# Performance work log

Hardware: AMD Instinct MI355X
Metric: run time of the kernel (lower is better)

Reference implementation:

```python
import jax, jax.numpy as jnp
import numpy as np
from jax import lax

LOG2PI = float(np.log(2.0 * np.pi))
N_K, N_T, N_C, N_D, N_SPK = 256, 128, 32, 10, 1000000

def _std_normal_logpdf(x):
    return -0.5 * (x * x + LOG2PI)

def _normal_logpdf(x, mu, log_sig):
    z = (x - mu) * jnp.exp(-log_sig)
    return -0.5 * (z * z + LOG2PI) - log_sig

def safe_log(x, minval=1e-10):
    return jnp.log(x + minval)

def setup_inputs() -> dict:
    key = jax.random.key(0)
    ks_ = jax.random.split(key, 8)
    s = jax.random.normal(ks_[0], (N_SPK, N_D), dtype=jnp.float32)
    y = jax.random.normal(ks_[1], (N_K, N_T), dtype=jnp.float32)
    ks = jax.random.randint(ks_[2], (N_SPK,), 0, N_K, dtype=jnp.int32)
    ts = jax.random.randint(ks_[3], (N_SPK,), 0, N_T, dtype=jnp.int32)
    means = jax.random.normal(ks_[4], (N_C, N_D), dtype=jnp.float32)
    A = jax.random.normal(ks_[5], (N_C, N_D, N_D), dtype=jnp.float32)
    covs = jnp.einsum('cij,ckj->cik', A, A) / N_D + jnp.eye(N_D, dtype=jnp.float32)
    b_mu = jax.random.normal(ks_[6], (N_C,), dtype=jnp.float32)
    b_log_sig = jax.random.normal(ks_[7], (N_C,), dtype=jnp.float32)
    beta_mu = jax.random.normal(jax.random.fold_in(key, 10), (N_C, N_T), dtype=jnp.float32)
    beta_log_sig = jax.random.normal(jax.random.fold_in(key, 11), (N_C, N_T), dtype=jnp.float32)
    return {"s": s, "y": y, "ks": ks, "ts": ts, "means": means, "covs": covs,
            "b_mu": b_mu, "b_log_sig": b_log_sig, "beta_mu": beta_mu, "beta_log_sig": beta_log_sig}

def _mvn_ll(s, means, covs):
    # ll[n, c] = MVN(means[c], covs[c]).log_prob(s[n]); loop over small n_c via lax.map
    L = jnp.linalg.cholesky(covs)                       # (c, d, d)
    logdet = 2.0 * jnp.sum(jnp.log(jnp.diagonal(L, axis1=1, axis2=2)), axis=1)  # (c,)
    d = s.shape[1]
    def comp(args):
        mu, Lc, ld = args
        diff = s - mu                                   # (n, d)
        z = jax.scipy.linalg.solve_triangular(Lc, diff.T, lower=True)  # (d, n)
        return -0.5 * (d * LOG2PI + ld + jnp.sum(z * z, axis=0))       # (n,)
    return lax.map(comp, (means, L, logdet)).T          # (n, c)

def reference(s, y, ks, ts, means, covs, b_mu, b_log_sig, beta_mu, beta_log_sig):
    # sampling=False path: use variational means
    b_sample, beta_sample = b_mu, beta_mu               # (c,), (c, t)
    # log_lambdas[k, c, t] = b[c] + beta[c, t] * y[k, t]
    log_lambdas = b_sample[None, :, None] + beta_sample[None, :, :] * y[:, None, :]
    log_pis = jax.nn.log_softmax(log_lambdas, axis=1)   # (k, c, t)
    ll = _mvn_ll(s, means, covs)                        # (n, c)
    logits = ll + log_pis[ks, :, ts]                    # per-spike gather -> (n, c)
    r = jax.nn.softmax(logits, axis=1)                  # responsibilities (n, c)
    log_prior = jnp.sum(_std_normal_logpdf(b_sample)) + jnp.sum(_std_normal_logpdf(beta_sample))
    log_q = jnp.sum(_normal_logpdf(b_sample, b_mu, b_log_sig)) + \
            jnp.sum(_normal_logpdf(beta_sample, beta_mu, beta_log_sig))
    elbo = log_prior - log_q
    elbo += jnp.sum(r * logits)
    elbo -= jnp.sum(r * safe_log(r))
    return elbo
```

## Files before the change

### kernel.cpp

```cpp
#include <hip/hip_runtime.h>
#include <hip/hip_bf16.h>
#include <math.h>

#define NK 256
#define NT 128
#define NC 32
#define ND 10
#define NSPK 1000000
#define LOG2PI 1.8378770664093453f
#define NCHUNK ((NSPK + 255) / 256)
#define GRID 1024

#define FSTR 36
#define LDS_DW (256 * FSTR)

typedef __attribute__((ext_vector_type(8))) short short8;
typedef __attribute__((ext_vector_type(4))) float floatx4;
typedef __attribute__((ext_vector_type(4))) int intx4;

union FragCvt { intx4 i; short8 s; };


__device__ inline unsigned pack_bf16(float a, float b) {
  __hip_bfloat16 ha = __float2bfloat16(a), hb = __float2bfloat16(b);
  unsigned short ua, ub;
  __builtin_memcpy(&ua, &ha, 2);
  __builtin_memcpy(&ub, &hb, 2);
  return (unsigned)ua | ((unsigned)ub << 16);
}

__global__ void prep_kernel(const float* __restrict__ y,
                            const float* __restrict__ means,
                            const float* __restrict__ covs,
                            const float* __restrict__ b_mu,
                            const float* __restrict__ b_ls,
                            const float* __restrict__ beta_mu,
                            const float* __restrict__ beta_ls,
                            int* __restrict__ wt,
                            float* __restrict__ cpack,
                            float* __restrict__ pisT,
                            double* __restrict__ acc,
                            unsigned int* __restrict__ counter) {
  int blk = blockIdx.x;
  int tid = threadIdx.x;

  if (blk == 0) {
    int c = tid;
    if (c >= NC) return;

    float M[ND][ND];
    #pragma unroll
    for (int i = 0; i < ND; ++i)
      #pragma unroll
      for (int j = 0; j < ND; ++j)
        M[i][j] = covs[c * ND * ND + i * ND + j];

    float logdet = 0.f;
    #pragma unroll
    for (int j = 0; j < ND; ++j) {
      float d = M[j][j];
      #pragma unroll
      for (int k = 0; k < ND; ++k) if (k < j) d -= M[j][k] * M[j][k];
      float sq = sqrtf(d);
      M[j][j] = sq;
      logdet += 2.f * __logf(sq);
      float inv = 1.f / sq;
      #pragma unroll
      for (int i = 0; i < ND; ++i) {
        if (i > j) {
          float s2 = M[i][j];
          #pragma unroll
          for (int k = 0; k < ND; ++k) if (k < j) s2 -= M[i][k] * M[j][k];
          M[i][j] = s2 * inv;
        }
      }
    }

    #pragma unroll
    for (int j = 0; j < ND; ++j) {
      M[j][j] = 1.f / M[j][j];
      #pragma unroll
      for (int i = 0; i < ND; ++i) {
        if (i > j) {
          float s2 = 0.f;
          #pragma unroll
          for (int k = 0; k < ND; ++k) if (k >= j && k < i) s2 += M[i][k] * M[k][j];
          M[i][j] = -s2 / M[i][i];
        }
      }
    }

    float pd[ND];
    #pragma unroll
    for (int i = 0; i < ND; ++i) {
      #pragma unroll
      for (int jj = 0; jj < ND; ++jj) {
        if (jj >= i) {
          float s2 = 0.f;
          #pragma unroll
          for (int k = 0; k < ND; ++k) if (k >= jj) s2 += M[k][i] * M[k][jj];
          if (jj > i) M[i][jj] = s2;
          else pd[i] = s2;
        }
      }
    }

    float mu[ND], q[ND];
    #pragma unroll
    for (int i = 0; i < ND; ++i) mu[i] = means[c * ND + i];
    float muPmu = 0.f;
    #pragma unroll
    for (int i = 0; i < ND; ++i) {
      float a2 = pd[i] * mu[i];
      #pragma unroll
      for (int j = 0; j < ND; ++j) {
        if (j < i) a2 += M[j][i] * mu[j];
        if (j > i) a2 += M[i][j] * mu[j];
      }
      q[i] = a2;
      muPmu += mu[i] * a2;
    }
    float cst = -0.5f * ((float)ND * LOG2PI + logdet + muPmu);

    float wv[64];
    int p = 0;
    #pragma unroll
    for (int i = 0; i < ND; ++i)
      #pragma unroll
      for (int j = 0; j < ND; ++j)
        if (j >= i && !(i == 9 && j == 9))
          wv[p++] = (i == j) ? -0.5f * pd[i] : -M[i][j];
    #pragma unroll
    for (int i = 0; i < ND; ++i) wv[54 + i] = q[i];

    #pragma unroll
    for (int j = 0; j < 32; ++j) {
      float a = wv[2 * j], b = wv[2 * j + 1];
      float ah = __bfloat162float(__float2bfloat16(a));
      float bh = __bfloat162float(__float2bfloat16(b));
      wt[c * 32 + j] = (int)pack_bf16(ah, bh);
      wt[(32 + c) * 32 + j] = (int)pack_bf16(a - ah, b - bh);
    }
    cpack[c] = cst;
    cpack[32 + c] = -0.5f * pd[9];

  } else if (blk == 1) {
    float local = 0.f;
    for (int i = tid; i < NC; i += 256)
      local += fmaf(-0.5f * b_mu[i], b_mu[i], b_ls[i]);
    for (int i = tid; i < NC * NT; i += 256)
      local += fmaf(-0.5f * beta_mu[i], beta_mu[i], beta_ls[i]);
    #pragma unroll
    for (int off = 32; off > 0; off >>= 1) local += __shfl_down(local, off);
    __shared__ float red[4];
    if ((tid & 63) == 0) red[tid >> 6] = local;
    __syncthreads();
    if (tid == 0) {
      acc[0] = (double)(red[0] + red[1] + red[2] + red[3]);
      counter[0] = 0u;
    }

  } else {
    int id = (blk - 2) * 256 + tid;
    int t = id & (NT - 1);
    float yv = y[id];
    float v[NC];
    float m = -1e30f;
    #pragma unroll
    for (int c = 0; c < NC; ++c) {
      v[c] = fmaf(beta_mu[c * NT + t], yv, b_mu[c]);
      m = fmaxf(m, v[c]);
    }
    float ssum = 0.f;
    #pragma unroll
    for (int c = 0; c < NC; ++c) ssum += __expf(v[c] - m);
    float lz = m + __logf(ssum);
    float* outp = pisT + (size_t)id * NC;
    #pragma unroll
    for (int c = 0; c < NC; ++c) outp[c] = v[c] - lz;
  }
}

__global__ __launch_bounds__(256, 4)
void spike_kernel(const float* __restrict__ s,
                  const int* __restrict__ ks,
                  const int* __restrict__ ts,
                  const int* __restrict__ wt,
                  const float* __restrict__ cpack,
                  const float* __restrict__ pisT,
                  double* __restrict__ acc,
                  unsigned int* __restrict__ counter,
                  float* __restrict__ out) {
  __shared__ int lds[LDS_DW];
  __shared__ float red[4];

  int tid = threadIdx.x;
  int wv_ = tid >> 6, L = tid & 63;
  int r = L & 15, q = L >> 4;

  FragCvt bf[2][2][2];
  #pragma unroll
  for (int h = 0; h < 2; ++h)
    #pragma unroll
    for (int nt = 0; nt < 2; ++nt)
      #pragma unroll
      for (int ks2 = 0; ks2 < 2; ++ks2)
        bf[h][nt][ks2].i =
            *(const intx4*)&wt[(h * 32 + nt * 16 + r) * 32 + ks2 * 16 + q * 4];

  float lse_sum = 0.f;

  for (int ci = blockIdx.x; ci < NCHUNK; ci += GRID) {
    int n = ci * 256 + tid;
    int nc = n < NSPK ? n : (NSPK - 1);

    const float2* srow = (const float2*)(s + (size_t)nc * ND);
    float sv[ND];
    #pragma unroll
    for (int i = 0; i < 5; ++i) {
      float2 v2 = srow[i];
      sv[2 * i] = v2.x;
      sv[2 * i + 1] = v2.y;
    }
    int kk_ = ks[nc], tt_ = ts[nc];

    float fv[64];
    {
      int p = 0;
      #pragma unroll
      for (int i = 0; i < ND; ++i)
        #pragma unroll
        for (int j = 0; j < ND; ++j)
          if (j >= i && !(i == 9 && j == 9)) fv[p++] = sv[i] * sv[j];
      #pragma unroll
      for (int i = 0; i < ND; ++i) fv[54 + i] = sv[i];
    }

    __syncthreads();
    {
      int rb = tid * FSTR;
      #pragma unroll
      for (int ch = 0; ch < 8; ++ch) {
        intx4 v;
        v.x = (int)pack_bf16(fv[8 * ch + 0], fv[8 * ch + 1]);
        v.y = (int)pack_bf16(fv[8 * ch + 2], fv[8 * ch + 3]);
        v.z = (int)pack_bf16(fv[8 * ch + 4], fv[8 * ch + 5]);
        v.w = (int)pack_bf16(fv[8 * ch + 6], fv[8 * ch + 7]);
        *(intx4*)&lds[rb + ch * 4] = v;
      }
    }
    __syncthreads();

    floatx4 accf[4][2];
    #pragma unroll
    for (int mt = 0; mt < 4; ++mt)
      #pragma unroll
      for (int nt = 0; nt < 2; ++nt)
        accf[mt][nt] = (floatx4){0.f, 0.f, 0.f, 0.f};

    #pragma unroll
    for (int mt = 0; mt < 4; ++mt) {
      #pragma unroll
      for (int ks2 = 0; ks2 < 2; ++ks2) {
        FragCvt a;
        a.i = *(const intx4*)&lds[(wv_ * 64 + mt * 16 + r) * FSTR + ks2 * 16 + q * 4];
        #pragma unroll
        for (int nt = 0; nt < 2; ++nt) {
          accf[mt][nt] = __builtin_amdgcn_mfma_f32_16x16x32_bf16(
              a.s, bf[0][nt][ks2].s, accf[mt][nt], 0, 0, 0);
          accf[mt][nt] = __builtin_amdgcn_mfma_f32_16x16x32_bf16(
              a.s, bf[1][nt][ks2].s, accf[mt][nt], 0, 0, 0);
        }
      }
    }

    const float4* lpp = (const float4*)(pisT + (size_t)(kk_ * NT + tt_) * NC);
    float4 lpv[8];
    #pragma unroll
    for (int i = 0; i < 8; ++i) lpv[i] = lpp[i];

    __syncthreads();

    #pragma unroll
    for (int mt = 0; mt < 4; ++mt)
      #pragma unroll
      for (int nt = 0; nt < 2; ++nt)
        #pragma unroll
        for (int rr = 0; rr < 4; ++rr) {
          int srow_ = wv_ * 64 + mt * 16 + q * 4 + rr;
          lds[srow_ * FSTR + nt * 16 + r] = __float_as_int(accf[mt][nt][rr]);
        }
    __syncthreads();

    {
      float lp[32];
      #pragma unroll
      for (int i = 0; i < 8; ++i) {
        lp[4 * i + 0] = lpv[i].x; lp[4 * i + 1] = lpv[i].y;
        lp[4 * i + 2] = lpv[i].z; lp[4 * i + 3] = lpv[i].w;
      }
      float s9sq = sv[9] * sv[9];
      int base = tid * FSTR;
      float lg[32];
      #pragma unroll
      for (int g = 0; g < 8; ++g) {
        intx4 lv = *(const intx4*)&lds[base + g * 4];
        lg[4 * g + 0] = __int_as_float(lv.x);
        lg[4 * g + 1] = __int_as_float(lv.y);
        lg[4 * g + 2] = __int_as_float(lv.z);
        lg[4 * g + 3] = __int_as_float(lv.w);
      }
      #pragma unroll
      for (int c = 0; c < 32; ++c)
        lg[c] += lp[c] + fmaf(cpack[32 + c], s9sq, cpack[c]);

      float m = lg[0];
      #pragma unroll
      for (int c = 1; c < 32; ++c) m = fmaxf(m, lg[c]);
      float ssum = 0.f;
      #pragma unroll
      for (int c = 0; c < 32; ++c) ssum += __expf(lg[c] - m);
      if (n < NSPK) lse_sum += m + __logf(ssum);
    }
  }

  #pragma unroll
  for (int off = 32; off > 0; off >>= 1) lse_sum += __shfl_down(lse_sum, off);
  if ((tid & 63) == 0) red[tid >> 6] = lse_sum;
  __syncthreads();
  if (tid == 0) {
    atomicAdd(acc, (double)(red[0] + red[1] + red[2] + red[3]));
    __threadfence();
    unsigned int old = atomicAdd(counter, 1u);
    if (old == GRID - 1) {
      __threadfence();
      double v = atomicAdd(acc, 0.0);
      out[0] = (float)v;
    }
  }
}

extern "C" void kernel_launch(void* const* d_in, const int* in_sizes, int n_in,
                              void* d_out, int out_size, void* d_ws, size_t ws_size,
                              hipStream_t stream) {
  const float* s       = (const float*)d_in[0];
  const float* y       = (const float*)d_in[1];
  const int*   ks      = (const int*)d_in[2];
  const int*   ts      = (const int*)d_in[3];
  const float* means   = (const float*)d_in[4];
  const float* covs    = (const float*)d_in[5];
  const float* b_mu    = (const float*)d_in[6];
  const float* b_ls    = (const float*)d_in[7];
  const float* beta_mu = (const float*)d_in[8];
  const float* beta_ls = (const float*)d_in[9];
  float* out = (float*)d_out;

  char* ws = (char*)d_ws;
  double* acc           = (double*)ws;
  unsigned int* counter = (unsigned int*)(ws + 8);
  float* cpack          = (float*)(ws + 64);
  int* wt               = (int*)(ws + 1024);
  float* pisT           = (float*)(ws + 16384);

  prep_kernel<<<2 + (NK * NT) / 256, 256, 0, stream>>>(
      y, means, covs, b_mu, b_ls, beta_mu, beta_ls, wt, cpack, pisT, acc, counter);
  spike_kernel<<<GRID, 256, 0, stream>>>(
      s, ks, ts, wt, cpack, pisT, acc, counter, out);
}
```

Before: 167.3 us.

## Use single-wave blocks without barriers and prefetch next chunk's spike data

Shrinks the spike kernel to 64-thread single-wavefront blocks with a 64-row LDS tile, so all __syncthreads calls and the cross-wave reduction go away. Each block now runs 4096 blocks over 64-spike chunks. It also software-pipelines the global loads: the next chunk's s, ks and ts are prefetched into registers during the current chunk's MFMA work, and the pisT gather is issued earlier, with sched_barriers fencing the phases. In exchange it issues more blocks and more global atomics, and it relies on lockstep execution within a wavefront to keep LDS access correct without barriers.

```diff
diff --git a/kernel.cpp b/kernel.cpp
--- a/kernel.cpp
+++ b/kernel.cpp
@@ -8,11 +8,12 @@
 #define ND 10
 #define NSPK 1000000
 #define LOG2PI 1.8378770664093453f
-#define NCHUNK ((NSPK + 255) / 256)
-#define GRID 1024
+
+#define NCH64 ((NSPK + 63) / 64)
+#define GRID2 4096
 
 #define FSTR 36
-#define LDS_DW (256 * FSTR)
+#define LDS_DW (64 * FSTR)
 
 typedef __attribute__((ext_vector_type(8))) short short8;
 typedef __attribute__((ext_vector_type(4))) float floatx4;
@@ -181,7 +182,7 @@
   }
 }
 
-__global__ __launch_bounds__(256, 4)
+__global__ __launch_bounds__(64, 4)
 void spike_kernel(const float* __restrict__ s,
                   const int* __restrict__ ks,
                   const int* __restrict__ ts,
@@ -192,11 +193,9 @@
                   unsigned int* __restrict__ counter,
                   float* __restrict__ out) {
   __shared__ int lds[LDS_DW];
-  __shared__ float red[4];
 
   int tid = threadIdx.x;
-  int wv_ = tid >> 6, L = tid & 63;
-  int r = L & 15, q = L >> 4;
+  int r = tid & 15, q = tid >> 4;
 
   FragCvt bf[2][2][2];
   #pragma unroll
@@ -204,25 +203,28 @@
     #pragma unroll
     for (int nt = 0; nt < 2; ++nt)
       #pragma unroll
-      for (int ks2 = 0; ks2 < 2; ++ks2)
-        bf[h][nt][ks2].i =
-            *(const intx4*)&wt[(h * 32 + nt * 16 + r) * 32 + ks2 * 16 + q * 4];
+      for (int k2 = 0; k2 < 2; ++k2)
+        bf[h][nt][k2].i =
+            *(const intx4*)&wt[(h * 32 + nt * 16 + r) * 32 + k2 * 16 + q * 4];
 
   float lse_sum = 0.f;
 
-  for (int ci = blockIdx.x; ci < NCHUNK; ci += GRID) {
-    int n = ci * 256 + tid;
+  int ci = blockIdx.x;
+  float4 sA, sB; float2 sC; int kk, tt;
+  {
+    int n = ci * 64 + tid;
     int nc = n < NSPK ? n : (NSPK - 1);
-
-    const float2* srow = (const float2*)(s + (size_t)nc * ND);
-    float sv[ND];
-    #pragma unroll
-    for (int i = 0; i < 5; ++i) {
-      float2 v2 = srow[i];
-      sv[2 * i] = v2.x;
-      sv[2 * i + 1] = v2.y;
-    }
-    int kk_ = ks[nc], tt_ = ts[nc];
+    const float* srow = s + (size_t)nc * ND;
+    sA = *(const float4*)srow;
+    sB = *(const float4*)(srow + 4);
+    sC = *(const float2*)(srow + 8);
+    kk = ks[nc]; tt = ts[nc];
+  }
+
+  for (; ci < NCH64; ci += GRID2) {
+    int n = ci * 64 + tid;
+    float sv[10] = {sA.x, sA.y, sA.z, sA.w, sB.x, sB.y, sB.z, sB.w, sC.x, sC.y};
+    float s9sq = sv[9] * sv[9];
 
     float fv[64];
     {
@@ -235,8 +237,6 @@
       #pragma unroll
       for (int i = 0; i < ND; ++i) fv[54 + i] = sv[i];
     }
-
-    __syncthreads();
     {
       int rb = tid * FSTR;
       #pragma unroll
@@ -249,7 +249,24 @@
         *(intx4*)&lds[rb + ch * 4] = v;
       }
     }
-    __syncthreads();
+
+    const float4* lpp = (const float4*)(pisT + (size_t)(kk * NT + tt) * NC);
+    float4 lpv[8];
+    #pragma unroll
+    for (int i = 0; i < 8; ++i) lpv[i] = lpp[i];
+
+    int cn = ci + GRID2;
+    if (cn < NCH64) {
+      int n2 = cn * 64 + tid;
+      int nc2 = n2 < NSPK ? n2 : (NSPK - 1);
+      const float* srow2 = s + (size_t)nc2 * ND;
+      sA = *(const float4*)srow2;
+      sB = *(const float4*)(srow2 + 4);
+      sC = *(const float2*)(srow2 + 8);
+      kk = ks[nc2]; tt = ts[nc2];
+    }
+
+    __builtin_amdgcn_sched_barrier(0);
 
     floatx4 accf[4][2];
     #pragma unroll
@@ -261,25 +278,20 @@
     #pragma unroll
     for (int mt = 0; mt < 4; ++mt) {
       #pragma unroll
-      for (int ks2 = 0; ks2 < 2; ++ks2) {
+      for (int k2 = 0; k2 < 2; ++k2) {
         FragCvt a;
-        a.i = *(const intx4*)&lds[(wv_ * 64 + mt * 16 + r) * FSTR + ks2 * 16 + q * 4];
+        a.i = *(const intx4*)&lds[(mt * 16 + r) * FSTR + k2 * 16 + q * 4];
         #pragma unroll
         for (int nt = 0; nt < 2; ++nt) {
           accf[mt][nt] = __builtin_amdgcn_mfma_f32_16x16x32_bf16(
-              a.s, bf[0][nt][ks2].s, accf[mt][nt], 0, 0, 0);
+              a.s, bf[0][nt][k2].s, accf[mt][nt], 0, 0, 0);
           accf[mt][nt] = __builtin_amdgcn_mfma_f32_16x16x32_bf16(
-              a.s, bf[1][nt][ks2].s, accf[mt][nt], 0, 0, 0);
-        }
-      }
-    }
-
-    const float4* lpp = (const float4*)(pisT + (size_t)(kk_ * NT + tt_) * NC);
-    float4 lpv[8];
-    #pragma unroll
-    for (int i = 0; i < 8; ++i) lpv[i] = lpp[i];
-
-    __syncthreads();
+              a.s, bf[1][nt][k2].s, accf[mt][nt], 0, 0, 0);
+        }
+      }
+    }
+
+    __builtin_amdgcn_sched_barrier(0);
 
     #pragma unroll
     for (int mt = 0; mt < 4; ++mt)
@@ -287,10 +299,11 @@
       for (int nt = 0; nt < 2; ++nt)
         #pragma unroll
         for (int rr = 0; rr < 4; ++rr) {
-          int srow_ = wv_ * 64 + mt * 16 + q * 4 + rr;
+          int srow_ = mt * 16 + q * 4 + rr;
           lds[srow_ * FSTR + nt * 16 + r] = __float_as_int(accf[mt][nt][rr]);
         }
-    __syncthreads();
+
+    __builtin_amdgcn_sched_barrier(0);
 
     {
       float lp[32];
@@ -299,7 +312,6 @@
         lp[4 * i + 0] = lpv[i].x; lp[4 * i + 1] = lpv[i].y;
         lp[4 * i + 2] = lpv[i].z; lp[4 * i + 3] = lpv[i].w;
       }
-      float s9sq = sv[9] * sv[9];
       int base = tid * FSTR;
       float lg[32];
       #pragma unroll
@@ -326,13 +338,11 @@
 
   #pragma unroll
   for (int off = 32; off > 0; off >>= 1) lse_sum += __shfl_down(lse_sum, off);
-  if ((tid & 63) == 0) red[tid >> 6] = lse_sum;
-  __syncthreads();
   if (tid == 0) {
-    atomicAdd(acc, (double)(red[0] + red[1] + red[2] + red[3]));
+    atomicAdd(acc, (double)lse_sum);
     __threadfence();
     unsigned int old = atomicAdd(counter, 1u);
-    if (old == GRID - 1) {
+    if (old == GRID2 - 1) {
       __threadfence();
       double v = atomicAdd(acc, 0.0);
       out[0] = (float)v;
@@ -364,6 +374,6 @@
 
   prep_kernel<<<2 + (NK * NT) / 256, 256, 0, stream>>>(
       y, means, covs, b_mu, b_ls, beta_mu, beta_ls, wt, cpack, pisT, acc, counter);
-  spike_kernel<<<GRID, 256, 0, stream>>>(
+  spike_kernel<<<GRID2, 64, 0, stream>>>(
       s, ks, ts, wt, cpack, pisT, acc, counter, out);
 }
```

Result: slower. 229.1 us (+36.9%).

## Prefetch next chunk's spike data, drop block barriers, tree-reduce logsumexp

Applied to the files above, without the earlier changes.

The next chunk's spike features and ks/ts indices are now loaded with nontemporal loads during the current iteration, and the log_pis gather is issued earlier, so global-memory latency overlaps with compute. All __syncthreads in the loop are removed, because each wave only reads and writes its own 64 LDS rows. The max and exp-sum over 32 components become tree and multi-accumulator reductions to shorten dependency chains. The gain comes from better latency hiding. The cost is more live registers, and correctness now relies on wave-local LDS ordering with no barrier.

```diff
diff --git a/kernel.cpp b/kernel.cpp
--- a/kernel.cpp
+++ b/kernel.cpp
@@ -16,6 +16,7 @@
 
 typedef __attribute__((ext_vector_type(8))) short short8;
 typedef __attribute__((ext_vector_type(4))) float floatx4;
+typedef __attribute__((ext_vector_type(2))) float floatx2;
 typedef __attribute__((ext_vector_type(4))) int intx4;
 
 union FragCvt { intx4 i; short8 s; };
@@ -204,25 +205,46 @@
     #pragma unroll
     for (int nt = 0; nt < 2; ++nt)
       #pragma unroll
-      for (int ks2 = 0; ks2 < 2; ++ks2)
-        bf[h][nt][ks2].i =
-            *(const intx4*)&wt[(h * 32 + nt * 16 + r) * 32 + ks2 * 16 + q * 4];
+      for (int k2 = 0; k2 < 2; ++k2)
+        bf[h][nt][k2].i =
+            *(const intx4*)&wt[(h * 32 + nt * 16 + r) * 32 + k2 * 16 + q * 4];
 
   float lse_sum = 0.f;
 
-  for (int ci = blockIdx.x; ci < NCHUNK; ci += GRID) {
+  int ci = blockIdx.x;
+  floatx4 sA, sB; floatx2 sC; int kk, tt;
+  {
     int n = ci * 256 + tid;
     int nc = n < NSPK ? n : (NSPK - 1);
-
-    const float2* srow = (const float2*)(s + (size_t)nc * ND);
-    float sv[ND];
-    #pragma unroll
-    for (int i = 0; i < 5; ++i) {
-      float2 v2 = srow[i];
-      sv[2 * i] = v2.x;
-      sv[2 * i + 1] = v2.y;
-    }
-    int kk_ = ks[nc], tt_ = ts[nc];
+    const float* srow = s + (size_t)nc * ND;
+    sA = __builtin_nontemporal_load((const floatx4*)srow);
+    sB = __builtin_nontemporal_load((const floatx4*)(srow + 4));
+    sC = __builtin_nontemporal_load((const floatx2*)(srow + 8));
+    kk = __builtin_nontemporal_load(ks + nc);
+    tt = __builtin_nontemporal_load(ts + nc);
+  }
+
+  for (; ci < NCHUNK; ci += GRID) {
+    int n = ci * 256 + tid;
+    float sv[10] = {sA.x, sA.y, sA.z, sA.w, sB.x, sB.y, sB.z, sB.w, sC.x, sC.y};
+    float s9sq = sv[9] * sv[9];
+
+    const float4* lpp = (const float4*)(pisT + (size_t)(kk * NT + tt) * NC);
+    float4 lpv[8];
+    #pragma unroll
+    for (int i = 0; i < 8; ++i) lpv[i] = lpp[i];
+
+    int cn = ci + GRID;
+    if (cn < NCHUNK) {
+      int n2 = cn * 256 + tid;
+      int nc2 = n2 < NSPK ? n2 : (NSPK - 1);
+      const float* srow2 = s + (size_t)nc2 * ND;
+      sA = __builtin_nontemporal_load((const floatx4*)srow2);
+      sB = __builtin_nontemporal_load((const floatx4*)(srow2 + 4));
+      sC = __builtin_nontemporal_load((const floatx2*)(srow2 + 8));
+      kk = __builtin_nontemporal_load(ks + nc2);
+      tt = __builtin_nontemporal_load(ts + nc2);
+    }
 
     float fv[64];
     {
@@ -235,8 +257,6 @@
       #pragma unroll
       for (int i = 0; i < ND; ++i) fv[54 + i] = sv[i];
     }
-
-    __syncthreads();
     {
       int rb = tid * FSTR;
       #pragma unroll
@@ -249,7 +269,6 @@
         *(intx4*)&lds[rb + ch * 4] = v;
       }
     }
-    __syncthreads();
 
     floatx4 accf[4][2];
     #pragma unroll
@@ -261,25 +280,18 @@
     #pragma unroll
     for (int mt = 0; mt < 4; ++mt) {
       #pragma unroll
-      for (int ks2 = 0; ks2 < 2; ++ks2) {
+      for (int k2 = 0; k2 < 2; ++k2) {
         FragCvt a;
-        a.i = *(const intx4*)&lds[(wv_ * 64 + mt * 16 + r) * FSTR + ks2 * 16 + q * 4];
+        a.i = *(const intx4*)&lds[(wv_ * 64 + mt * 16 + r) * FSTR + k2 * 16 + q * 4];
         #pragma unroll
         for (int nt = 0; nt < 2; ++nt) {
           accf[mt][nt] = __builtin_amdgcn_mfma_f32_16x16x32_bf16(
-              a.s, bf[0][nt][ks2].s, accf[mt][nt], 0, 0, 0);
+              a.s, bf[0][nt][k2].s, accf[mt][nt], 0, 0, 0);
           accf[mt][nt] = __builtin_amdgcn_mfma_f32_16x16x32_bf16(
-              a.s, bf[1][nt][ks2].s, accf[mt][nt], 0, 0, 0);
-        }
-      }
-    }
-
-    const float4* lpp = (const float4*)(pisT + (size_t)(kk_ * NT + tt_) * NC);
-    float4 lpv[8];
-    #pragma unroll
-    for (int i = 0; i < 8; ++i) lpv[i] = lpp[i];
-
-    __syncthreads();
+              a.s, bf[1][nt][k2].s, accf[mt][nt], 0, 0, 0);
+        }
+      }
+    }
 
     #pragma unroll
     for (int mt = 0; mt < 4; ++mt)
@@ -290,7 +302,6 @@
           int srow_ = wv_ * 64 + mt * 16 + q * 4 + rr;
           lds[srow_ * FSTR + nt * 16 + r] = __float_as_int(accf[mt][nt][rr]);
         }
-    __syncthreads();
 
     {
       float lp[32];
@@ -299,7 +310,6 @@
         lp[4 * i + 0] = lpv[i].x; lp[4 * i + 1] = lpv[i].y;
         lp[4 * i + 2] = lpv[i].z; lp[4 * i + 3] = lpv[i].w;
       }
-      float s9sq = sv[9] * sv[9];
       int base = tid * FSTR;
       float lg[32];
       #pragma unroll
@@ -314,12 +324,26 @@
       for (int c = 0; c < 32; ++c)
         lg[c] += lp[c] + fmaf(cpack[32 + c], s9sq, cpack[c]);
 
-      float m = lg[0];
-      #pragma unroll
-      for (int c = 1; c < 32; ++c) m = fmaxf(m, lg[c]);
-      float ssum = 0.f;
-      #pragma unroll
-      for (int c = 0; c < 32; ++c) ssum += __expf(lg[c] - m);
+      float m16[16];
+      #pragma unroll
+      for (int c = 0; c < 16; ++c) m16[c] = fmaxf(lg[c], lg[c + 16]);
+      float m8[8];
+      #pragma unroll
+      for (int c = 0; c < 8; ++c) m8[c] = fmaxf(m16[c], m16[c + 8]);
+      float m4[4];
+      #pragma unroll
+      for (int c = 0; c < 4; ++c) m4[c] = fmaxf(m8[c], m8[c + 4]);
+      float m = fmaxf(fmaxf(m4[0], m4[1]), fmaxf(m4[2], m4[3]));
+
+      float ss0 = 0.f, ss1 = 0.f, ss2 = 0.f, ss3 = 0.f;
+      #pragma unroll
+      for (int c = 0; c < 8; ++c) {
+        ss0 += __expf(lg[4 * c + 0] - m);
+        ss1 += __expf(lg[4 * c + 1] - m);
+        ss2 += __expf(lg[4 * c + 2] - m);
+        ss3 += __expf(lg[4 * c + 3] - m);
+      }
+      float ssum = (ss0 + ss1) + (ss2 + ss3);
       if (n < NSPK) lse_sum += m + __logf(ssum);
     }
   }
```

After: 170.8 us. +2.1%, slower.
